# Kernel optimization log

Hardware: AMD Instinct MI355X
Metric: run time of the kernel (lower is better)

## Reference

```python
import jax, jax.numpy as jnp
import numpy as np

B, T, D, H = 256, 512, 128, 256  # batch, frames, input_dim, hidden_size


def _lstm_cell(x, h, c, Wih, Whh, bih, bhh):
    # PyTorch gate order: i, f, g, o
    gates = x @ Wih.T + h @ Whh.T + bih + bhh  # [B, 4H]
    i, f, g, o = jnp.split(gates, 4, axis=-1)
    c_new = jax.nn.sigmoid(f) * c + jax.nn.sigmoid(i) * jnp.tanh(g)
    h_new = jax.nn.sigmoid(o) * jnp.tanh(c_new)
    return h_new, c_new


def setup_inputs() -> dict:
    key = jax.random.key(0)
    k = 1.0 / np.sqrt(H)

    def rnd(i, shape):
        return jax.random.uniform(jax.random.fold_in(key, i), shape,
                                  dtype=jnp.float32, minval=-k, maxval=k)

    inp = {"x": jax.random.normal(jax.random.fold_in(key, 0), (B, T, D), dtype=jnp.float32)}
    i = 1
    for pre in ("e", "d"):
        for l in (0, 1):
            in_dim = D if l == 0 else H
            inp[f"{pre}_Wih{l}"] = rnd(i, (4 * H, in_dim)); i += 1
            inp[f"{pre}_Whh{l}"] = rnd(i, (4 * H, H)); i += 1
            inp[f"{pre}_bih{l}"] = rnd(i, (4 * H,)); i += 1
            inp[f"{pre}_bhh{l}"] = rnd(i, (4 * H,)); i += 1
    inp["fc_W"] = rnd(i, (D, H)); i += 1
    inp["fc_b"] = rnd(i, (D,))
    return inp


def reference(x,
              e_Wih0, e_Whh0, e_bih0, e_bhh0,
              e_Wih1, e_Whh1, e_bih1, e_bhh1,
              d_Wih0, d_Whh0, d_bih0, d_bhh0,
              d_Wih1, d_Whh1, d_bih1, d_bhh1,
              fc_W, fc_b):
    b, t, d = x.shape
    h = e_Whh0.shape[1]
    z = jnp.zeros((b, h), x.dtype)

    # ---- encoder: 2-layer LSTM over time, keep only final (h, c) states ----
    def enc_step(carry, xt):
        h1, c1, h2, c2 = carry
        h1, c1 = _lstm_cell(xt, h1, c1, e_Wih0, e_Whh0, e_bih0, e_bhh0)
        h2, c2 = _lstm_cell(h1, h2, c2, e_Wih1, e_Whh1, e_bih1, e_bhh1)
        return (h1, c1, h2, c2), None

    en_state, _ = jax.lax.scan(enc_step, (z, z, z, z), jnp.swapaxes(x, 0, 1))

    def dec_step(carry, _):
        inp, h1, c1, h2, c2 = carry
        h1, c1 = _lstm_cell(inp, h1, c1, d_Wih0, d_Whh0, d_bih0, d_bhh0)
        h2, c2 = _lstm_cell(h1, h2, c2, d_Wih1, d_Whh1, d_bih1, d_bhh1)
        y = h2 @ fc_W.T + fc_b  # [B, D]
        return (y, h1, c1, h2, c2), y

    init = (jnp.zeros((b, d), x.dtype),) + en_state
    _, ys = jax.lax.scan(dec_step, init, None, length=t)
    return jnp.swapaxes(ys, 0, 1)  # [B, T, D]
```

## Files before the change

### kernel.cpp

```cpp
#include <hip/hip_runtime.h>
#include <stddef.h>

#define BB 256
#define TT 512
#define DD 128
#define HH 256

__device__ __forceinline__ float sigm(float x)  { return 1.0f / (1.0f + __expf(-x)); }
__device__ __forceinline__ float tanh_(float x) { return 2.0f / (1.0f + __expf(-2.0f * x)) - 1.0f; }

template<int K1, int XMODE>
__global__ __launch_bounds__(BB) void cell_kernel(
    const float* __restrict__ xsrc, int t,
    const float* __restrict__ hin, const float* __restrict__ cin,
    const float* __restrict__ Wih, const float* __restrict__ Whh,
    const float* __restrict__ bih, const float* __restrict__ bhh,
    float* __restrict__ hout, float* __restrict__ cout_)
{
    const int j = blockIdx.x;
    const int b = threadIdx.x;

    float a0 = bih[j]        + bhh[j];
    float a1 = bih[HH + j]   + bhh[HH + j];
    float a2 = bih[2*HH + j] + bhh[2*HH + j];
    float a3 = bih[3*HH + j] + bhh[3*HH + j];

    const float* __restrict__ wi0 = Wih + (size_t)(0*HH + j) * K1;
    const float* __restrict__ wi1 = Wih + (size_t)(1*HH + j) * K1;
    const float* __restrict__ wi2 = Wih + (size_t)(2*HH + j) * K1;
    const float* __restrict__ wi3 = Wih + (size_t)(3*HH + j) * K1;

    #pragma unroll 4
    for (int k = 0; k < K1; ++k) {
        float xv = (XMODE == 0) ? xsrc[(size_t)b * TT * DD + (size_t)t * DD + k]
                                : xsrc[k * BB + b];
        a0 = fmaf(xv, wi0[k], a0);
        a1 = fmaf(xv, wi1[k], a1);
        a2 = fmaf(xv, wi2[k], a2);
        a3 = fmaf(xv, wi3[k], a3);
    }

    const float* __restrict__ wh0 = Whh + (size_t)(0*HH + j) * HH;
    const float* __restrict__ wh1 = Whh + (size_t)(1*HH + j) * HH;
    const float* __restrict__ wh2 = Whh + (size_t)(2*HH + j) * HH;
    const float* __restrict__ wh3 = Whh + (size_t)(3*HH + j) * HH;

    #pragma unroll 4
    for (int k = 0; k < HH; ++k) {
        float hv = hin[k * BB + b];
        a0 = fmaf(hv, wh0[k], a0);
        a1 = fmaf(hv, wh1[k], a1);
        a2 = fmaf(hv, wh2[k], a2);
        a3 = fmaf(hv, wh3[k], a3);
    }

    float ig = sigm(a0);
    float fg = sigm(a1);
    float gg = tanh_(a2);
    float og = sigm(a3);

    float cn = fg * cin[j * BB + b] + ig * gg;
    cout_[j * BB + b] = cn;
    hout[j * BB + b]  = og * tanh_(cn);
}

__global__ __launch_bounds__(BB) void fc_kernel(
    const float* __restrict__ h2, const float* __restrict__ W,
    const float* __restrict__ bias, float* __restrict__ ybuf,
    float* __restrict__ out, int t)
{
    const int d = blockIdx.x;
    const int b = threadIdx.x;

    float acc = bias[d];
    const float* __restrict__ w = W + (size_t)d * HH;
    #pragma unroll 4
    for (int j = 0; j < HH; ++j)
        acc = fmaf(h2[j * BB + b], w[j], acc);

    ybuf[d * BB + b] = acc;
    out[(size_t)b * TT * DD + (size_t)t * DD + d] = acc;
}

__global__ __launch_bounds__(256) void zero_kernel(float* __restrict__ p, int n)
{
    int i = blockIdx.x * 256 + threadIdx.x;
    if (i < n) p[i] = 0.0f;
}

extern "C" void kernel_launch(void* const* d_in, const int* in_sizes, int n_in,
                              void* d_out, int out_size, void* d_ws, size_t ws_size,
                              hipStream_t stream)
{
    const float* x       = (const float*)d_in[0];
    const float* e_Wih0  = (const float*)d_in[1];
    const float* e_Whh0  = (const float*)d_in[2];
    const float* e_bih0  = (const float*)d_in[3];
    const float* e_bhh0  = (const float*)d_in[4];
    const float* e_Wih1  = (const float*)d_in[5];
    const float* e_Whh1  = (const float*)d_in[6];
    const float* e_bih1  = (const float*)d_in[7];
    const float* e_bhh1  = (const float*)d_in[8];
    const float* d_Wih0  = (const float*)d_in[9];
    const float* d_Whh0  = (const float*)d_in[10];
    const float* d_bih0  = (const float*)d_in[11];
    const float* d_bhh0  = (const float*)d_in[12];
    const float* d_Wih1  = (const float*)d_in[13];
    const float* d_Whh1  = (const float*)d_in[14];
    const float* d_bih1  = (const float*)d_in[15];
    const float* d_bhh1  = (const float*)d_in[16];
    const float* fc_W    = (const float*)d_in[17];
    const float* fc_b    = (const float*)d_in[18];

    float* out = (float*)d_out;

    float* ws   = (float*)d_ws;
    const int S = HH * BB;
    float* h1[2] = { ws + 0 * S, ws + 1 * S };
    float* h2[2] = { ws + 2 * S, ws + 3 * S };
    float* c1    = ws + 4 * S;
    float* c2    = ws + 5 * S;
    float* ybuf  = ws + 6 * S;
    const int total_state = 6 * S + DD * BB;

    zero_kernel<<<(total_state + 255) / 256, 256, 0, stream>>>(ws, total_state);

    for (int t = 0; t < TT; ++t) {
        const int pr = t & 1, pw = 1 - pr;
        cell_kernel<DD, 0><<<HH, BB, 0, stream>>>(
            x, t, h1[pr], c1, e_Wih0, e_Whh0, e_bih0, e_bhh0, h1[pw], c1);
        cell_kernel<HH, 1><<<HH, BB, 0, stream>>>(
            h1[pw], 0, h2[pr], c2, e_Wih1, e_Whh1, e_bih1, e_bhh1, h2[pw], c2);
    }

    for (int s = 0; s < TT; ++s) {
        const int pr = s & 1, pw = 1 - pr;
        cell_kernel<DD, 1><<<HH, BB, 0, stream>>>(
            ybuf, 0, h1[pr], c1, d_Wih0, d_Whh0, d_bih0, d_bhh0, h1[pw], c1);
        cell_kernel<HH, 1><<<HH, BB, 0, stream>>>(
            h1[pw], 0, h2[pr], c2, d_Wih1, d_Whh1, d_bih1, d_bhh1, h2[pw], c2);
        fc_kernel<<<DD, BB, 0, stream>>>(h2[pw], fc_W, fc_b, ybuf, out, s);
    }
}
```

Measured before the change: 62.59 ms.

## Replace per-step kernel launches with persistent cooperative kernel and folded decoder input

Replaces roughly 2,500 small per-timestep kernel launches with one persistent cooperative kernel. Cell state is kept in registers, each of 8 batch groups synchronizes through its own atomic barrier, and each wave splits the K reduction across half-waves joined by a shuffle. It also precomputes M = d_Wih0·fc_W and its bias, so the decoder's fed-back fc output is folded into the layer-0 recurrence and fc sits off the critical path. The aim is to remove launch overhead and global round-trips of c state, at the cost of spin-barrier latency per step and a dependence on all 512 workgroups being co-resident.

Result: slower. 228.4 ms (+264.9%).

```diff
diff --git a/kernel.cpp b/kernel.cpp
--- a/kernel.cpp
+++ b/kernel.cpp
@@ -1,85 +1,273 @@
 #include <hip/hip_runtime.h>
 #include <stddef.h>
+#include <stdint.h>
 
 #define BB 256
 #define TT 512
 #define DD 128
 #define HH 256
 
+#define NGROUP 8
+#define WG_PER_GROUP 64
+#define NWG (NGROUP * WG_PER_GROUP)
+
 __device__ __forceinline__ float sigm(float x)  { return 1.0f / (1.0f + __expf(-x)); }
 __device__ __forceinline__ float tanh_(float x) { return 2.0f / (1.0f + __expf(-2.0f * x)) - 1.0f; }
 
-template<int K1, int XMODE>
-__global__ __launch_bounds__(BB) void cell_kernel(
-    const float* __restrict__ xsrc, int t,
-    const float* __restrict__ hin, const float* __restrict__ cin,
-    const float* __restrict__ Wih, const float* __restrict__ Whh,
-    const float* __restrict__ bih, const float* __restrict__ bhh,
-    float* __restrict__ hout, float* __restrict__ cout_)
-{
-    const int j = blockIdx.x;
-    const int b = threadIdx.x;
-
-    float a0 = bih[j]        + bhh[j];
-    float a1 = bih[HH + j]   + bhh[HH + j];
-    float a2 = bih[2*HH + j] + bhh[2*HH + j];
-    float a3 = bih[3*HH + j] + bhh[3*HH + j];
-
-    const float* __restrict__ wi0 = Wih + (size_t)(0*HH + j) * K1;
-    const float* __restrict__ wi1 = Wih + (size_t)(1*HH + j) * K1;
-    const float* __restrict__ wi2 = Wih + (size_t)(2*HH + j) * K1;
-    const float* __restrict__ wi3 = Wih + (size_t)(3*HH + j) * K1;
-
-    #pragma unroll 4
-    for (int k = 0; k < K1; ++k) {
-        float xv = (XMODE == 0) ? xsrc[(size_t)b * TT * DD + (size_t)t * DD + k]
-                                : xsrc[k * BB + b];
-        a0 = fmaf(xv, wi0[k], a0);
-        a1 = fmaf(xv, wi1[k], a1);
-        a2 = fmaf(xv, wi2[k], a2);
-        a3 = fmaf(xv, wi3[k], a3);
-    }
-
-    const float* __restrict__ wh0 = Whh + (size_t)(0*HH + j) * HH;
-    const float* __restrict__ wh1 = Whh + (size_t)(1*HH + j) * HH;
-    const float* __restrict__ wh2 = Whh + (size_t)(2*HH + j) * HH;
-    const float* __restrict__ wh3 = Whh + (size_t)(3*HH + j) * HH;
-
-    #pragma unroll 4
-    for (int k = 0; k < HH; ++k) {
-        float hv = hin[k * BB + b];
-        a0 = fmaf(hv, wh0[k], a0);
-        a1 = fmaf(hv, wh1[k], a1);
-        a2 = fmaf(hv, wh2[k], a2);
-        a3 = fmaf(hv, wh3[k], a3);
-    }
-
-    float ig = sigm(a0);
-    float fg = sigm(a1);
-    float gg = tanh_(a2);
-    float og = sigm(a3);
-
-    float cn = fg * cin[j * BB + b] + ig * gg;
-    cout_[j * BB + b] = cn;
-    hout[j * BB + b]  = og * tanh_(cn);
-}
-
-__global__ __launch_bounds__(BB) void fc_kernel(
-    const float* __restrict__ h2, const float* __restrict__ W,
-    const float* __restrict__ bias, float* __restrict__ ybuf,
-    float* __restrict__ out, int t)
-{
-    const int d = blockIdx.x;
-    const int b = threadIdx.x;
-
-    float acc = bias[d];
-    const float* __restrict__ w = W + (size_t)d * HH;
-    #pragma unroll 4
-    for (int j = 0; j < HH; ++j)
-        acc = fmaf(h2[j * BB + b], w[j], acc);
-
-    ybuf[d * BB + b] = acc;
-    out[(size_t)b * TT * DD + (size_t)t * DD + d] = acc;
+__device__ __forceinline__ void group_barrier(unsigned int* cnt, unsigned int* gen)
+{
+    __syncthreads();
+    if (threadIdx.x == 0) {
+        __threadfence();
+        unsigned int g   = __hip_atomic_load(gen, __ATOMIC_RELAXED, __HIP_MEMORY_SCOPE_AGENT);
+        unsigned int old = __hip_atomic_fetch_add(cnt, 1u, __ATOMIC_ACQ_REL, __HIP_MEMORY_SCOPE_AGENT);
+        if (old == (unsigned int)(WG_PER_GROUP - 1)) {
+            __hip_atomic_store(cnt, 0u, __ATOMIC_RELAXED, __HIP_MEMORY_SCOPE_AGENT);
+            __hip_atomic_fetch_add(gen, 1u, __ATOMIC_RELEASE, __HIP_MEMORY_SCOPE_AGENT);
+        } else {
+            while (__hip_atomic_load(gen, __ATOMIC_ACQUIRE, __HIP_MEMORY_SCOPE_AGENT) == g)
+                __builtin_amdgcn_s_sleep(2);
+        }
+    }
+    __syncthreads();
+    __threadfence();
+}
+
+__device__ __forceinline__ void dot4(const float* __restrict__ w0, const float* __restrict__ w1,
+                                     const float* __restrict__ w2, const float* __restrict__ w3,
+                                     const float* __restrict__ hb, int k0, int k1,
+                                     float& a0, float& a1, float& a2, float& a3)
+{
+    #pragma unroll 8
+    for (int k = k0; k < k1; ++k) {
+        const float hv = hb[k * 256];
+        a0 = fmaf(w0[k], hv, a0);
+        a1 = fmaf(w1[k], hv, a1);
+        a2 = fmaf(w2[k], hv, a2);
+        a3 = fmaf(w3[k], hv, a3);
+    }
+}
+
+__device__ __forceinline__ void dotx(const float* __restrict__ w0, const float* __restrict__ w1,
+                                     const float* __restrict__ w2, const float* __restrict__ w3,
+                                     const float* __restrict__ xp, int n,
+                                     float& a0, float& a1, float& a2, float& a3)
+{
+    #pragma unroll 8
+    for (int k = 0; k < n; ++k) {
+        const float xv = xp[k];
+        a0 = fmaf(w0[k], xv, a0);
+        a1 = fmaf(w1[k], xv, a1);
+        a2 = fmaf(w2[k], xv, a2);
+        a3 = fmaf(w3[k], xv, a3);
+    }
+}
+
+__global__ __launch_bounds__(256, 2) void lstm_ae_persistent(
+    const float* __restrict__ x,
+    const float* __restrict__ eWih0, const float* __restrict__ eWhh0,
+    const float* __restrict__ ebih0, const float* __restrict__ ebhh0,
+    const float* __restrict__ eWih1, const float* __restrict__ eWhh1,
+    const float* __restrict__ ebih1, const float* __restrict__ ebhh1,
+    const float* __restrict__ dWhh0, const float* __restrict__ dbih0, const float* __restrict__ dbhh0,
+    const float* __restrict__ dWih1, const float* __restrict__ dWhh1,
+    const float* __restrict__ dbih1, const float* __restrict__ dbhh1,
+    const float* __restrict__ Mm,   const float* __restrict__ bM,
+    const float* __restrict__ fcW,  const float* __restrict__ fcb,
+    float* __restrict__ h1a, float* __restrict__ h1b,
+    float* __restrict__ h2a, float* __restrict__ h2b,
+    unsigned int* __restrict__ bar,
+    float* __restrict__ out)
+{
+    const int wg = blockIdx.x;
+    const int g  = wg & 7;
+    const int m  = wg >> 3;
+    const int w  = __builtin_amdgcn_readfirstlane((int)(threadIdx.x >> 6));
+    const int lane = (int)(threadIdx.x & 63);
+    const int kh = lane >> 5;
+    const int b  = lane & 31;
+    const int u  = __builtin_amdgcn_readfirstlane(m * 4 + w);
+    const int bg = g * 32 + b;
+
+    unsigned int* cnt = bar + g * 16;
+    unsigned int* gen = bar + 128 + g * 16;
+
+    const int r0 = u, r1 = HH + u, r2 = 2*HH + u, r3 = 3*HH + u;
+
+    const float* exw0 = eWih0 + (size_t)r0 * DD;
+    const float* exw1 = eWih0 + (size_t)r1 * DD;
+    const float* exw2 = eWih0 + (size_t)r2 * DD;
+    const float* exw3 = eWih0 + (size_t)r3 * DD;
+    const float* ehw0 = eWhh0 + (size_t)r0 * HH;
+    const float* ehw1 = eWhh0 + (size_t)r1 * HH;
+    const float* ehw2 = eWhh0 + (size_t)r2 * HH;
+    const float* ehw3 = eWhh0 + (size_t)r3 * HH;
+    const float* e1x0 = eWih1 + (size_t)r0 * HH;
+    const float* e1x1 = eWih1 + (size_t)r1 * HH;
+    const float* e1x2 = eWih1 + (size_t)r2 * HH;
+    const float* e1x3 = eWih1 + (size_t)r3 * HH;
+    const float* e1h0 = eWhh1 + (size_t)r0 * HH;
+    const float* e1h1 = eWhh1 + (size_t)r1 * HH;
+    const float* e1h2 = eWhh1 + (size_t)r2 * HH;
+    const float* e1h3 = eWhh1 + (size_t)r3 * HH;
+    const float* M0   = Mm    + (size_t)r0 * HH;
+    const float* M1   = Mm    + (size_t)r1 * HH;
+    const float* M2   = Mm    + (size_t)r2 * HH;
+    const float* M3   = Mm    + (size_t)r3 * HH;
+    const float* d0h0 = dWhh0 + (size_t)r0 * HH;
+    const float* d0h1 = dWhh0 + (size_t)r1 * HH;
+    const float* d0h2 = dWhh0 + (size_t)r2 * HH;
+    const float* d0h3 = dWhh0 + (size_t)r3 * HH;
+    const float* d1x0 = dWih1 + (size_t)r0 * HH;
+    const float* d1x1 = dWih1 + (size_t)r1 * HH;
+    const float* d1x2 = dWih1 + (size_t)r2 * HH;
+    const float* d1x3 = dWih1 + (size_t)r3 * HH;
+    const float* d1h0 = dWhh1 + (size_t)r0 * HH;
+    const float* d1h1 = dWhh1 + (size_t)r1 * HH;
+    const float* d1h2 = dWhh1 + (size_t)r2 * HH;
+    const float* d1h3 = dWhh1 + (size_t)r3 * HH;
+
+    const float eb0_0 = ebih0[r0] + ebhh0[r0];
+    const float eb0_1 = ebih0[r1] + ebhh0[r1];
+    const float eb0_2 = ebih0[r2] + ebhh0[r2];
+    const float eb0_3 = ebih0[r3] + ebhh0[r3];
+    const float eb1_0 = ebih1[r0] + ebhh1[r0];
+    const float eb1_1 = ebih1[r1] + ebhh1[r1];
+    const float eb1_2 = ebih1[r2] + ebhh1[r2];
+    const float eb1_3 = ebih1[r3] + ebhh1[r3];
+    const float db0_0 = dbih0[r0] + dbhh0[r0];
+    const float db0_1 = dbih0[r1] + dbhh0[r1];
+    const float db0_2 = dbih0[r2] + dbhh0[r2];
+    const float db0_3 = dbih0[r3] + dbhh0[r3];
+    const float db1_0 = dbih1[r0] + dbhh1[r0];
+    const float db1_1 = dbih1[r1] + dbhh1[r1];
+    const float db1_2 = dbih1[r2] + dbhh1[r2];
+    const float db1_3 = dbih1[r3] + dbhh1[r3];
+    const float bM0 = bM[r0], bM1 = bM[r1], bM2 = bM[r2], bM3 = bM[r3];
+
+    float c1 = 0.f, c2 = 0.f;
+    float* h1buf[2] = { h1a, h1b };
+    float* h2buf[2] = { h2a, h2b };
+    const int hidx = u * 256 + bg;
+
+    for (int t = 0; t < TT; ++t) {
+        const int p = t & 1;
+        const float* h1p = h1buf[p] + bg;
+        const float* h2p = h2buf[p] + bg;
+        float* h1n = h1buf[p ^ 1];
+        float* h2n = h2buf[p ^ 1];
+
+        float a0 = 0.f, a1 = 0.f, a2 = 0.f, a3 = 0.f;
+        if (kh == 0) {
+            const float* xp = x + (size_t)bg * (TT * DD) + (size_t)t * DD;
+            dotx(exw0, exw1, exw2, exw3, xp, DD, a0, a1, a2, a3);
+            dot4(ehw0, ehw1, ehw2, ehw3, h1p, 0, 64, a0, a1, a2, a3);
+        } else {
+            dot4(ehw0, ehw1, ehw2, ehw3, h1p, 64, 256, a0, a1, a2, a3);
+        }
+        a0 += __shfl_xor(a0, 32); a1 += __shfl_xor(a1, 32);
+        a2 += __shfl_xor(a2, 32); a3 += __shfl_xor(a3, 32);
+        a0 += eb0_0; a1 += eb0_1; a2 += eb0_2; a3 += eb0_3;
+        c1 = sigm(a1) * c1 + sigm(a0) * tanh_(a2);
+        {
+            float hv = sigm(a3) * tanh_(c1);
+            if (lane < 32) h1n[hidx] = hv;
+        }
+        group_barrier(cnt, gen);
+
+        a0 = 0.f; a1 = 0.f; a2 = 0.f; a3 = 0.f;
+        if (kh == 0) dot4(e1x0, e1x1, e1x2, e1x3, h1n + bg, 0, 256, a0, a1, a2, a3);
+        else         dot4(e1h0, e1h1, e1h2, e1h3, h2p,      0, 256, a0, a1, a2, a3);
+        a0 += __shfl_xor(a0, 32); a1 += __shfl_xor(a1, 32);
+        a2 += __shfl_xor(a2, 32); a3 += __shfl_xor(a3, 32);
+        a0 += eb1_0; a1 += eb1_1; a2 += eb1_2; a3 += eb1_3;
+        c2 = sigm(a1) * c2 + sigm(a0) * tanh_(a2);
+        {
+            float hv = sigm(a3) * tanh_(c2);
+            if (lane < 32) h2n[hidx] = hv;
+        }
+        group_barrier(cnt, gen);
+    }
+
+    for (int s = 0; s < TT; ++s) {
+        const int p = s & 1;
+        const float* h1p = h1buf[p] + bg;
+        const float* h2p = h2buf[p] + bg;
+        float* h1n = h1buf[p ^ 1];
+        float* h2n = h2buf[p ^ 1];
+
+        float a0 = 0.f, a1 = 0.f, a2 = 0.f, a3 = 0.f;
+        if (kh == 0) {
+            if (s > 0) dot4(M0, M1, M2, M3, h2p, 0, 256, a0, a1, a2, a3);
+        } else {
+            dot4(d0h0, d0h1, d0h2, d0h3, h1p, 0, 256, a0, a1, a2, a3);
+        }
+        a0 += __shfl_xor(a0, 32); a1 += __shfl_xor(a1, 32);
+        a2 += __shfl_xor(a2, 32); a3 += __shfl_xor(a3, 32);
+        a0 += db0_0; a1 += db0_1; a2 += db0_2; a3 += db0_3;
+        if (s > 0) { a0 += bM0; a1 += bM1; a2 += bM2; a3 += bM3; }
+        c1 = sigm(a1) * c1 + sigm(a0) * tanh_(a2);
+        {
+            float hv = sigm(a3) * tanh_(c1);
+            if (lane < 32) h1n[hidx] = hv;
+        }
+        group_barrier(cnt, gen);
+
+        a0 = 0.f; a1 = 0.f; a2 = 0.f; a3 = 0.f;
+        if (kh == 0) dot4(d1x0, d1x1, d1x2, d1x3, h1n + bg, 0, 256, a0, a1, a2, a3);
+        else         dot4(d1h0, d1h1, d1h2, d1h3, h2p,      0, 256, a0, a1, a2, a3);
+        a0 += __shfl_xor(a0, 32); a1 += __shfl_xor(a1, 32);
+        a2 += __shfl_xor(a2, 32); a3 += __shfl_xor(a3, 32);
+        a0 += db1_0; a1 += db1_1; a2 += db1_2; a3 += db1_3;
+        c2 = sigm(a1) * c2 + sigm(a0) * tanh_(a2);
+        {
+            float hv = sigm(a3) * tanh_(c2);
+            if (lane < 32) h2n[hidx] = hv;
+        }
+        group_barrier(cnt, gen);
+
+        if (w < 2) {
+            const int d = __builtin_amdgcn_readfirstlane(2 * m + w);
+            const float* fr = fcW + (size_t)d * HH;
+            const float* hq = h2n + bg;
+            float acc = 0.f;
+            const int k0 = kh * 128, k1 = k0 + 128;
+            #pragma unroll 8
+            for (int k = k0; k < k1; ++k)
+                acc = fmaf(fr[k], hq[k * 256], acc);
+            acc += __shfl_xor(acc, 32);
+            acc += fcb[d];
+            if (kh == 0)
+                out[(size_t)bg * (TT * DD) + (size_t)s * DD + d] = acc;
+        }
+    }
+}
+
+__global__ __launch_bounds__(256) void prep_M(const float* __restrict__ Wih_d0,
+                                              const float* __restrict__ fcW,
+                                              float* __restrict__ Mm)
+{
+    const int r = blockIdx.x;
+    const int j = threadIdx.x;
+    float acc = 0.f;
+    #pragma unroll 8
+    for (int d = 0; d < DD; ++d)
+        acc = fmaf(Wih_d0[(size_t)r * DD + d], fcW[(size_t)d * HH + j], acc);
+    Mm[(size_t)r * HH + j] = acc;
+}
+
+__global__ __launch_bounds__(256) void prep_bM(const float* __restrict__ Wih_d0,
+                                               const float* __restrict__ fcb,
+                                               float* __restrict__ bM)
+{
+    const int r = blockIdx.x * 256 + threadIdx.x;
+    if (r < 4 * HH) {
+        float acc = 0.f;
+        #pragma unroll 8
+        for (int d = 0; d < DD; ++d)
+            acc = fmaf(Wih_d0[(size_t)r * DD + d], fcb[d], acc);
+        bM[r] = acc;
+    }
 }
 
 __global__ __launch_bounds__(256) void zero_kernel(float* __restrict__ p, int n)
@@ -111,34 +299,34 @@
     const float* d_bhh1  = (const float*)d_in[16];
     const float* fc_W    = (const float*)d_in[17];
     const float* fc_b    = (const float*)d_in[18];
-
     float* out = (float*)d_out;
 
-    float* ws   = (float*)d_ws;
-    const int S = HH * BB;
-    float* h1[2] = { ws + 0 * S, ws + 1 * S };
-    float* h2[2] = { ws + 2 * S, ws + 3 * S };
-    float* c1    = ws + 4 * S;
-    float* c2    = ws + 5 * S;
-    float* ybuf  = ws + 6 * S;
-    const int total_state = 6 * S + DD * BB;
-
-    zero_kernel<<<(total_state + 255) / 256, 256, 0, stream>>>(ws, total_state);
-
-    for (int t = 0; t < TT; ++t) {
-        const int pr = t & 1, pw = 1 - pr;
-        cell_kernel<DD, 0><<<HH, BB, 0, stream>>>(
-            x, t, h1[pr], c1, e_Wih0, e_Whh0, e_bih0, e_bhh0, h1[pw], c1);
-        cell_kernel<HH, 1><<<HH, BB, 0, stream>>>(
-            h1[pw], 0, h2[pr], c2, e_Wih1, e_Whh1, e_bih1, e_bhh1, h2[pw], c2);
-    }
-
-    for (int s = 0; s < TT; ++s) {
-        const int pr = s & 1, pw = 1 - pr;
-        cell_kernel<DD, 1><<<HH, BB, 0, stream>>>(
-            ybuf, 0, h1[pr], c1, d_Wih0, d_Whh0, d_bih0, d_bhh0, h1[pw], c1);
-        cell_kernel<HH, 1><<<HH, BB, 0, stream>>>(
-            h1[pw], 0, h2[pr], c2, d_Wih1, d_Whh1, d_bih1, d_bhh1, h2[pw], c2);
-        fc_kernel<<<DD, BB, 0, stream>>>(h2[pw], fc_W, fc_b, ybuf, out, s);
-    }
-}
+    float* ws = (float*)d_ws;
+    unsigned int* bar = (unsigned int*)ws;
+    float* h1a = ws + 1024;
+    float* h1b = ws + 66560;
+    float* h2a = ws + 132096;
+    float* h2b = ws + 197632;
+    float* Mm  = ws + 263168;
+    float* bM  = ws + 525312;
+    const int zero_n = 263168;
+
+    zero_kernel<<<(zero_n + 255) / 256, 256, 0, stream>>>(ws, zero_n);
+    prep_M<<<4 * HH, 256, 0, stream>>>(d_Wih0, fc_W, Mm);
+    prep_bM<<<4, 256, 0, stream>>>(d_Wih0, fc_b, bM);
+
+    void* args[] = {
+        (void*)&x,
+        (void*)&e_Wih0, (void*)&e_Whh0, (void*)&e_bih0, (void*)&e_bhh0,
+        (void*)&e_Wih1, (void*)&e_Whh1, (void*)&e_bih1, (void*)&e_bhh1,
+        (void*)&d_Whh0, (void*)&d_bih0, (void*)&d_bhh0,
+        (void*)&d_Wih1, (void*)&d_Whh1, (void*)&d_bih1, (void*)&d_bhh1,
+        (void*)&Mm, (void*)&bM,
+        (void*)&fc_W, (void*)&fc_b,
+        (void*)&h1a, (void*)&h1b, (void*)&h2a, (void*)&h2b,
+        (void*)&bar,
+        (void*)&out
+    };
+    hipLaunchCooperativeKernel((const void*)lstm_ae_persistent,
+                               dim3(NWG), dim3(256), args, 0, stream);
+}
```
